# Kernel tuning notes

Hardware: AMD Instinct MI355X
Metric: run time of the kernel (lower is better)

## Reference

```python
import jax, jax.numpy as jnp
import numpy as np

N_NODES = 100000
N_EDGES = 3200000
NUM_FEATURES = 5
HIDDEN = 64


def _gcn_layer(x, W, b, src, dst, norm, n_nodes):
    """One GCNConv: out = scatter_add(norm * (xW)[src] -> dst) + b.
    src/dst/norm already include self-loops and symmetric normalization."""
    h = x @ W                                  # [N, out_ch] small dense GEMM
    msg = h[src] * norm[:, None]               # [E+N, out_ch] gather + scale
    out = jax.ops.segment_sum(msg, dst, num_segments=n_nodes)
    return out + b


def _build_norm(edge_index, n_nodes):
    """Add self-loops, compute D^{-1/2}[src] * D^{-1/2}[dst] (GCN symmetric norm)."""
    loop = jnp.arange(n_nodes, dtype=edge_index.dtype)
    src = jnp.concatenate([edge_index[0], loop])
    dst = jnp.concatenate([edge_index[1], loop])
    deg = jax.ops.segment_sum(jnp.ones_like(dst, dtype=jnp.float32), dst,
                              num_segments=n_nodes)
    dis = jnp.where(deg > 0, jax.lax.rsqrt(deg), 0.0)  # deg^{-1/2}
    norm = dis[src] * dis[dst]
    return src, dst, norm


def setup_inputs() -> dict:
    key = jax.random.key(0)
    ks = jax.random.split(key, 8)
    x = jax.random.normal(ks[0], (N_NODES, NUM_FEATURES), dtype=jnp.float32)
    edge_index = jax.random.randint(ks[1], (2, N_EDGES), 0, N_NODES, dtype=jnp.int64)
    # glorot-ish scaled params
    W1 = jax.random.normal(ks[2], (NUM_FEATURES, HIDDEN), dtype=jnp.float32) * (1.0 / np.sqrt(NUM_FEATURES))
    b1 = jnp.zeros((HIDDEN,), dtype=jnp.float32)
    W2 = jax.random.normal(ks[3], (HIDDEN, HIDDEN), dtype=jnp.float32) * (1.0 / np.sqrt(HIDDEN))
    b2 = jnp.zeros((HIDDEN,), dtype=jnp.float32)
    W3 = jax.random.normal(ks[4], (HIDDEN, 1), dtype=jnp.float32) * (1.0 / np.sqrt(HIDDEN))
    b3 = jnp.zeros((1,), dtype=jnp.float32)
    return {"x": x, "edge_index": edge_index,
            "W1": W1, "b1": b1, "W2": W2, "b2": b2, "W3": W3, "b3": b3}


def reference(x, edge_index, W1, b1, W2, b2, W3, b3):
    n_nodes = x.shape[0]
    src, dst, norm = _build_norm(edge_index, n_nodes)
    h = jax.nn.relu(_gcn_layer(x, W1, b1, src, dst, norm, n_nodes))
    h = jax.nn.relu(_gcn_layer(h, W2, b2, src, dst, norm, n_nodes))
    out = _gcn_layer(h, W3, b3, src, dst, norm, n_nodes)  # [N, 1]
    return out
```

## Files before the change

kernel.cpp:

```cpp
#include <hip/hip_runtime.h>
#include <hip/hip_fp16.h>

#define NFEAT 5
#define HID 64
#define BSH 9
#define BNODES 512
#define MAXBK 256
#define CHUNK 4096

__global__ void k_binit(int* bcur, int ecap) {
    bcur[threadIdx.x] = threadIdx.x * ecap;
}

__global__ __launch_bounds__(256) void
k_bin(const int* __restrict__ src, const int* __restrict__ dst,
      int* bcur, int2* __restrict__ binned, int E) {
    __shared__ int2 stg[CHUNK];
    __shared__ int hist[MAXBK], base[MAXBK], gb[MAXBK];
    int t = threadIdx.x;
    int e0 = blockIdx.x * CHUNK;
    int cc = E - e0; if (cc > CHUNK) cc = CHUNK;
    hist[t] = 0;
    __syncthreads();
    int2 my[CHUNK / 256]; int mb[CHUNK / 256]; int mr[CHUNK / 256];
#pragma unroll
    for (int k = 0; k < CHUNK / 256; ++k) {
        int i = e0 + k * 256 + t;
        if (i < E) {
            my[k].x = src[i]; my[k].y = dst[i];
            mb[k] = my[k].y >> BSH;
            mr[k] = atomicAdd(&hist[mb[k]], 1);
        } else mb[k] = -1;
    }
    __syncthreads();
    int c = hist[t];
    base[t] = c;
    __syncthreads();
    for (int off = 1; off < 256; off <<= 1) {
        int a = (t >= off) ? base[t - off] : 0;
        __syncthreads();
        base[t] += a;
        __syncthreads();
    }
    base[t] -= c;
    gb[t] = c ? atomicAdd(&bcur[t], c) : 0;
    __syncthreads();
#pragma unroll
    for (int k = 0; k < CHUNK / 256; ++k)
        if (mb[k] >= 0) stg[base[mb[k]] + mr[k]] = my[k];
    __syncthreads();
#pragma unroll
    for (int k = 0; k < CHUNK / 256; ++k) {
        int p = k * 256 + t;
        if (p < cc) {
            int2 v = stg[p];
            int b = v.y >> BSH;
            binned[gb[b] + (p - base[b])] = v;
        }
    }
}

__global__ __launch_bounds__(256) void
k_sort(const int2* __restrict__ binned, const int* __restrict__ bcur,
       const float* __restrict__ x, int* __restrict__ rpN, int* __restrict__ rpE,
       int* __restrict__ csr, float* __restrict__ dis, float* __restrict__ xs,
       int n, int ecap) {
    __shared__ int hist[BNODES];
    __shared__ int cur[BNODES];
    __shared__ int tmp[256];
    int t = threadIdx.x, b = blockIdx.x;
    int e0 = b * ecap;
    int e1 = bcur[b];
    int v0 = b << BSH;
    int nv = n - v0; if (nv > BNODES) nv = BNODES;
    hist[t] = 0; hist[t + 256] = 0;
    __syncthreads();
    for (int i = e0 + t; i < e1; i += 256) {
        int2 ed = binned[i];
        atomicAdd(&hist[ed.y - v0], 1);
    }
    __syncthreads();
    for (int vl = t; vl < nv; vl += 256) {
        int v = v0 + vl;
        float dv = rsqrtf((float)hist[vl] + 1.0f);
        dis[v] = dv;
        const float* xr = x + (size_t)v * NFEAT;
        float* xw = xs + (size_t)v * 8;
        xw[0] = dv * xr[0]; xw[1] = dv * xr[1]; xw[2] = dv * xr[2];
        xw[3] = dv * xr[3]; xw[4] = dv * xr[4];
        xw[5] = 0.f; xw[6] = 0.f; xw[7] = 0.f;
    }
    int b0 = t * 2;
    int c0 = hist[b0], c1 = hist[b0 + 1];
    int s = c0 + c1;
    tmp[t] = s;
    __syncthreads();
    for (int off = 1; off < 256; off <<= 1) {
        int a = (t >= off) ? tmp[t - off] : 0;
        __syncthreads();
        tmp[t] += a;
        __syncthreads();
    }
    int excl = e0 + tmp[t] - s;
    cur[b0] = excl;
    cur[b0 + 1] = excl + c0;
    if (b0 < nv)     { rpN[v0 + b0]     = excl;      rpE[v0 + b0]     = excl + c0; }
    if (b0 + 1 < nv) { rpN[v0 + b0 + 1] = excl + c0; rpE[v0 + b0 + 1] = excl + c0 + c1; }
    __syncthreads();
    for (int i = e0 + t; i < e1; i += 256) {
        int2 ed = binned[i];
        int pos = atomicAdd(&cur[ed.y - v0], 1);
        csr[pos] = ed.x;
    }
}

__global__ __launch_bounds__(256) void
k_layer1(const int* __restrict__ rpN, const int* __restrict__ rpE,
         const int* __restrict__ csr, const float* __restrict__ xs,
         const float* __restrict__ dis, const float* __restrict__ W1,
         const float* __restrict__ b1, __half* __restrict__ g1h, int n) {
    int wave = (blockIdx.x * blockDim.x + threadIdx.x) >> 6;
    int lane = threadIdx.x & 63;
    if (wave >= n) return;
    int v = wave;
    int r0 = rpN[v], r1 = rpE[v];
    float a0 = 0.f, a1 = 0.f, a2 = 0.f, a3 = 0.f, a4 = 0.f;
    for (int j = r0 + lane; j < r1; j += 64) {
        const float4* q = (const float4*)(xs + (size_t)csr[j] * 8);
        float4 qa = q[0], qb = q[1];
        a0 += qa.x; a1 += qa.y; a2 += qa.z; a3 += qa.w; a4 += qb.x;
    }
#pragma unroll
    for (int m = 32; m > 0; m >>= 1) {
        a0 += __shfl_xor(a0, m, 64); a1 += __shfl_xor(a1, m, 64);
        a2 += __shfl_xor(a2, m, 64); a3 += __shfl_xor(a3, m, 64);
        a4 += __shfl_xor(a4, m, 64);
    }
    float dv = dis[v];
    const float* pv = xs + (size_t)v * 8;
    a0 = dv * (a0 + pv[0]); a1 = dv * (a1 + pv[1]); a2 = dv * (a2 + pv[2]);
    a3 = dv * (a3 + pv[3]); a4 = dv * (a4 + pv[4]);
    int c = lane;
    float h = b1[c] + a0 * W1[c] + a1 * W1[64 + c] + a2 * W1[128 + c]
            + a3 * W1[192 + c] + a4 * W1[256 + c];
    g1h[(size_t)v * HID + c] = __float2half(dv * fmaxf(h, 0.0f));
}

__global__ __launch_bounds__(256) void
k_layer23(const int* __restrict__ rpN, const int* __restrict__ rpE,
          const int* __restrict__ csr, const __half* __restrict__ g1h,
          const float* __restrict__ dis, const float* __restrict__ W2,
          const float* __restrict__ b2, const float* __restrict__ W3,
          float* __restrict__ svs, int n) {
    __shared__ float W2s[HID * HID];
    for (int i = threadIdx.x; i < HID * HID; i += 256) W2s[i] = W2[i];
    __syncthreads();
    int wave = (blockIdx.x * blockDim.x + threadIdx.x) >> 6;
    int lane = threadIdx.x & 63;
    if (wave >= n) return;
    int v = wave;
    int r0 = rpN[v], r1 = rpE[v];
    float acc = __half2float(g1h[(size_t)v * HID + lane]);
    int j = r0;
    for (; j + 8 <= r1; j += 8) {
        int s0 = csr[j],     s1 = csr[j + 1], s2 = csr[j + 2], s3 = csr[j + 3];
        int s4 = csr[j + 4], s5 = csr[j + 5], s6 = csr[j + 6], s7 = csr[j + 7];
        float t0 = __half2float(g1h[(size_t)s0 * HID + lane]);
        float t1 = __half2float(g1h[(size_t)s1 * HID + lane]);
        float t2 = __half2float(g1h[(size_t)s2 * HID + lane]);
        float t3 = __half2float(g1h[(size_t)s3 * HID + lane]);
        float t4 = __half2float(g1h[(size_t)s4 * HID + lane]);
        float t5 = __half2float(g1h[(size_t)s5 * HID + lane]);
        float t6 = __half2float(g1h[(size_t)s6 * HID + lane]);
        float t7 = __half2float(g1h[(size_t)s7 * HID + lane]);
        acc += ((t0 + t1) + (t2 + t3)) + ((t4 + t5) + (t6 + t7));
    }
    for (; j < r1; ++j) acc += __half2float(g1h[(size_t)csr[j] * HID + lane]);
    float dv = dis[v];
    acc *= dv;
    float out = b2[lane];
#pragma unroll
    for (int k = 0; k < HID; ++k)
        out = fmaf(__shfl(acc, k, 64), W2s[(k << 6) + lane], out);
    out = fmaxf(out, 0.0f);
    float val = out * W3[lane];
#pragma unroll
    for (int m = 32; m > 0; m >>= 1) val += __shfl_xor(val, m, 64);
    if (lane == 0) svs[v] = dv * val;
}

__global__ __launch_bounds__(256) void
k_out(const int* __restrict__ rpN, const int* __restrict__ rpE,
      const int* __restrict__ csr, const float* __restrict__ svs,
      const float* __restrict__ dis, const float* __restrict__ b3,
      float* __restrict__ out, int n) {
    int wave = (blockIdx.x * blockDim.x + threadIdx.x) >> 6;
    int lane = threadIdx.x & 63;
    if (wave >= n) return;
    int v = wave;
    int r0 = rpN[v], r1 = rpE[v];
    float acc = (lane == 0) ? svs[v] : 0.f;
    for (int j = r0 + lane; j < r1; j += 64) acc += svs[csr[j]];
#pragma unroll
    for (int m = 32; m > 0; m >>= 1) acc += __shfl_xor(acc, m, 64);
    if (lane == 0) out[v] = b3[0] + dis[v] * acc;
}

extern "C" void kernel_launch(void* const* d_in, const int* in_sizes, int n_in,
                              void* d_out, int out_size, void* d_ws, size_t ws_size,
                              hipStream_t stream) {
    const float* x  = (const float*)d_in[0];
    const int*   ei = (const int*)d_in[1];
    const float* W1 = (const float*)d_in[2];
    const float* b1 = (const float*)d_in[3];
    const float* W2 = (const float*)d_in[4];
    const float* b2 = (const float*)d_in[5];
    const float* W3 = (const float*)d_in[6];
    const float* b3 = (const float*)d_in[7];
    float* out = (float*)d_out;

    const int n = out_size;
    const int E = in_sizes[1] / 2;
    const int* src = ei;
    const int* dst = ei + E;

    const int nbk  = (n + BNODES - 1) / BNODES;
    int ecap = E / nbk;
    ecap += ecap / 8 + 1024;

    int*    bcur   = (int*)d_ws;
    int*    rpN    = bcur + 512;
    int*    rpE    = rpN + n;
    float*  dis    = (float*)(rpE + n);
    float*  svs    = dis + n;
    int*    csr    = (int*)(svs + n);
    int2*   binned = (int2*)(csr + (size_t)nbk * ecap);
    float*  xs     = (float*)(binned + (size_t)nbk * ecap);
    __half* g1h    = (__half*)binned;

    const int B = 256;
    const int nchunk = (E + CHUNK - 1) / CHUNK;
    const int gridW  = ((size_t)n * 64 + B - 1) / B;

    k_binit  <<<1, 256, 0, stream>>>(bcur, ecap);
    k_bin    <<<nchunk, 256, 0, stream>>>(src, dst, bcur, binned, E);
    k_sort   <<<nbk, 256, 0, stream>>>(binned, bcur, x, rpN, rpE, csr, dis, xs, n, ecap);
    k_layer1 <<<gridW, B, 0, stream>>>(rpN, rpE, csr, xs, dis, W1, b1, g1h, n);
    k_layer23<<<gridW, B, 0, stream>>>(rpN, rpE, csr, g1h, dis, W2, b2, W3, svs, n);
    k_out    <<<gridW, B, 0, stream>>>(rpN, rpE, csr, svs, dis, b3, out, n);
}
```

Baseline: 378.7 us.

## Pack binned edges into 32-bit words and reuse first-pass ranks in sort

Binned edges are packed as a single 32-bit word (17-bit source plus local destination) instead of an int2, halving the intermediate traffic written by the bin kernel and read twice by the sort kernel. The sort kernel records each edge's rank from the histogram atomics in a shared-memory array, so the scatter pass needs no second round of shared atomics. The packing assumes node ids fit in 17 bits, and ecap is clamped to a fixed shared-memory capacity, which could silently drop edges if a bucket overflows. The larger shared-memory footprint may also lower occupancy of the sort kernel.

```diff
diff --git a/kernel.cpp b/kernel.cpp
--- a/kernel.cpp
+++ b/kernel.cpp
@@ -7,6 +7,7 @@
 #define BNODES 512
 #define MAXBK 256
 #define CHUNK 4096
+#define ECAPMAX 20480
 
 __global__ void k_binit(int* bcur, int ecap) {
     bcur[threadIdx.x] = threadIdx.x * ecap;
@@ -14,21 +15,23 @@
 
 __global__ __launch_bounds__(256) void
 k_bin(const int* __restrict__ src, const int* __restrict__ dst,
-      int* bcur, int2* __restrict__ binned, int E) {
-    __shared__ int2 stg[CHUNK];
+      int* bcur, unsigned* __restrict__ binned, int E) {
+    __shared__ unsigned stg[CHUNK];
+    __shared__ unsigned char bkt[CHUNK];
     __shared__ int hist[MAXBK], base[MAXBK], gb[MAXBK];
     int t = threadIdx.x;
     int e0 = blockIdx.x * CHUNK;
     int cc = E - e0; if (cc > CHUNK) cc = CHUNK;
     hist[t] = 0;
     __syncthreads();
-    int2 my[CHUNK / 256]; int mb[CHUNK / 256]; int mr[CHUNK / 256];
+    unsigned me[CHUNK / 256]; int mb[CHUNK / 256]; int mr[CHUNK / 256];
 #pragma unroll
     for (int k = 0; k < CHUNK / 256; ++k) {
         int i = e0 + k * 256 + t;
         if (i < E) {
-            my[k].x = src[i]; my[k].y = dst[i];
-            mb[k] = my[k].y >> BSH;
+            int s = src[i], d = dst[i];
+            mb[k] = d >> BSH;
+            me[k] = (unsigned)s | ((unsigned)(d & (BNODES - 1)) << 17);
             mr[k] = atomicAdd(&hist[mb[k]], 1);
         } else mb[k] = -1;
     }
@@ -47,37 +50,42 @@
     __syncthreads();
 #pragma unroll
     for (int k = 0; k < CHUNK / 256; ++k)
-        if (mb[k] >= 0) stg[base[mb[k]] + mr[k]] = my[k];
+        if (mb[k] >= 0) {
+            int p = base[mb[k]] + mr[k];
+            stg[p] = me[k];
+            bkt[p] = (unsigned char)mb[k];
+        }
     __syncthreads();
 #pragma unroll
     for (int k = 0; k < CHUNK / 256; ++k) {
         int p = k * 256 + t;
         if (p < cc) {
-            int2 v = stg[p];
-            int b = v.y >> BSH;
-            binned[gb[b] + (p - base[b])] = v;
+            int b = bkt[p];
+            binned[gb[b] + (p - base[b])] = stg[p];
         }
     }
 }
 
 __global__ __launch_bounds__(256) void
-k_sort(const int2* __restrict__ binned, const int* __restrict__ bcur,
+k_sort(const unsigned* __restrict__ binned, const int* __restrict__ bcur,
        const float* __restrict__ x, int* __restrict__ rpN, int* __restrict__ rpE,
        int* __restrict__ csr, float* __restrict__ dis, float* __restrict__ xs,
        int n, int ecap) {
+    __shared__ unsigned short rank[ECAPMAX];
     __shared__ int hist[BNODES];
     __shared__ int cur[BNODES];
     __shared__ int tmp[256];
     int t = threadIdx.x, b = blockIdx.x;
     int e0 = b * ecap;
-    int e1 = bcur[b];
+    int cnt = bcur[b] - e0;
+    if (cnt > ecap) cnt = ecap;
     int v0 = b << BSH;
     int nv = n - v0; if (nv > BNODES) nv = BNODES;
     hist[t] = 0; hist[t + 256] = 0;
     __syncthreads();
-    for (int i = e0 + t; i < e1; i += 256) {
-        int2 ed = binned[i];
-        atomicAdd(&hist[ed.y - v0], 1);
+    for (int i = t; i < cnt; i += 256) {
+        int vl = binned[e0 + i] >> 17;
+        rank[i] = (unsigned short)atomicAdd(&hist[vl], 1);
     }
     __syncthreads();
     for (int vl = t; vl < nv; vl += 256) {
@@ -107,10 +115,10 @@
     if (b0 < nv)     { rpN[v0 + b0]     = excl;      rpE[v0 + b0]     = excl + c0; }
     if (b0 + 1 < nv) { rpN[v0 + b0 + 1] = excl + c0; rpE[v0 + b0 + 1] = excl + c0 + c1; }
     __syncthreads();
-    for (int i = e0 + t; i < e1; i += 256) {
-        int2 ed = binned[i];
-        int pos = atomicAdd(&cur[ed.y - v0], 1);
-        csr[pos] = ed.x;
+    for (int i = t; i < cnt; i += 256) {
+        unsigned e = binned[e0 + i];
+        int vl = e >> 17;
+        csr[cur[vl] + rank[i]] = (int)(e & 0x1FFFF);
     }
 }
 
@@ -224,19 +232,20 @@
     const int* src = ei;
     const int* dst = ei + E;
 
-    const int nbk  = (n + BNODES - 1) / BNODES;
+    const int nbk = (n + BNODES - 1) / BNODES;
     int ecap = E / nbk;
     ecap += ecap / 8 + 1024;
-
-    int*    bcur   = (int*)d_ws;
-    int*    rpN    = bcur + 512;
-    int*    rpE    = rpN + n;
-    float*  dis    = (float*)(rpE + n);
-    float*  svs    = dis + n;
-    int*    csr    = (int*)(svs + n);
-    int2*   binned = (int2*)(csr + (size_t)nbk * ecap);
-    float*  xs     = (float*)(binned + (size_t)nbk * ecap);
-    __half* g1h    = (__half*)binned;
+    if (ecap > ECAPMAX) ecap = ECAPMAX;
+
+    int*      bcur   = (int*)d_ws;
+    int*      rpN    = bcur + 512;
+    int*      rpE    = rpN + n;
+    float*    dis    = (float*)(rpE + n);
+    float*    svs    = dis + n;
+    int*      csr    = (int*)(svs + n);
+    unsigned* binned = (unsigned*)(csr + (size_t)nbk * ecap);
+    float*    xs     = (float*)(binned + (size_t)nbk * ecap);
+    __half*   g1h    = (__half*)binned;
 
     const int B = 256;
     const int nchunk = (E + CHUNK - 1) / CHUNK;
```

After: 371.7 us. Within noise of the previous version (-1.9%).
